# Performance work log

Hardware: AMD Instinct MI355X
Metric: run time of the kernel (lower is better)

Reference implementation:

```python
import jax, jax.numpy as jnp
import numpy as np

EPS = 1e-8


def setup_inputs() -> dict:
    key = jax.random.key(0)
    k1, k2, k3 = jax.random.split(key, 3)
    K_, M, N = 2048, 512, 64
    x = jax.random.normal(k1, (K_, M), dtype=jnp.float32)
    w_att = jax.random.uniform(k2, (M, M), dtype=jnp.float32)
    w_b = jax.random.uniform(k3, (M, N), dtype=jnp.float32)
    return {"x": x, "w_att": w_att, "w_b": w_b, "l": 8}


def reference(x, w_att, w_b, l):
    # soft attention scores over features: [k, m]
    scores_soft = jax.nn.softmax(x @ w_att, axis=-1) + EPS
    # per-target l-th largest value of w_b over the m axis -> threshold [n]
    thr = jax.lax.top_k(w_b.T, l)[0][:, -1]  # [n]
    sh = w_b - thr[None, :] + EPS  # [m, n]
    # training-phase soft hard-mask: clamp to [-1, 1], shift to [0, 1]
    scores_hard = (jnp.clip(sh, -1.0, 1.0) + 1.0) * 0.5  # [m, n]
    # outer-product combine: 'mn,km->kmn' then 'kmn,km->kmn'
    mask_weight = scores_hard[None, :, :] * scores_soft[:, :, None]  # [k, m, n]
    out = mask_weight * x[:, :, None]  # [k, m, n]
    return out, scores_hard, scores_soft, mask_weight
```

## Files before the change

kernel.cpp:

```cpp
#include <hip/hip_runtime.h>
#include <math.h>

#define K_DIM 2048
#define M_DIM 512
#define N_DIM 64
#define EPSF 1e-8f
#define ROWS 8
#define TPB 512

typedef float f32x4 __attribute__((ext_vector_type(4)));

__global__ __launch_bounds__(256) void thr_hard_kernel(
    const float* __restrict__ w_b, const int* __restrict__ lptr,
    float* __restrict__ scores_hard) {
  __shared__ float col[M_DIM];
  __shared__ float red[256];
  const int n = blockIdx.x;
  const int t = threadIdx.x;
  const int L = lptr[0];

  col[t]       = w_b[t * N_DIM + n];
  col[t + 256] = w_b[(t + 256) * N_DIM + n];
  __syncthreads();

  const float v0 = col[t], v1 = col[t + 256];
  int c0 = 0, c1 = 0;
  for (int i = 0; i < M_DIM; ++i) {
    const float c = col[i];
    c0 += (c > v0);
    c1 += (c > v1);
  }
  float cand0 = (c0 <= L - 1) ? v0 : INFINITY;
  float cand1 = (c1 <= L - 1) ? v1 : INFINITY;
  red[t] = fminf(cand0, cand1);
  __syncthreads();
  for (int s = 128; s > 0; s >>= 1) {
    if (t < s) red[t] = fminf(red[t], red[t + s]);
    __syncthreads();
  }
  const float thr = red[0];

  {
    float sh0 = (col[t] - thr) + EPSF;
    float sh1 = (col[t + 256] - thr) + EPSF;
    sh0 = fminf(fmaxf(sh0, -1.0f), 1.0f);
    sh1 = fminf(fmaxf(sh1, -1.0f), 1.0f);
    scores_hard[t * N_DIM + n]         = (sh0 + 1.0f) * 0.5f;
    scores_hard[(t + 256) * N_DIM + n] = (sh1 + 1.0f) * 0.5f;
  }
}

__global__ __launch_bounds__(TPB) void fused_kernel(
    const float* __restrict__ x, const float* __restrict__ w,
    const float* __restrict__ hard, float* __restrict__ soft,
    f32x4* __restrict__ out, f32x4* __restrict__ mw) {
  __shared__ float xs[ROWS][M_DIM];
  __shared__ float sm[ROWS][M_DIM];
  const int t = threadIdx.x;
  const int k0 = blockIdx.x * ROWS;

  {
    const f32x4* xg = (const f32x4*)(x + (size_t)k0 * M_DIM);
    f32x4* xsv = (f32x4*)&xs[0][0];
    xsv[t]       = xg[t];
    xsv[t + TPB] = xg[t + TPB];
  }
  __syncthreads();

  {
    const int half = t >> 8;
    const int j0 = t & 255;
    const int r0 = half * 4;
    float acc[4][2];
#pragma unroll
    for (int r = 0; r < 4; ++r) { acc[r][0] = 0.0f; acc[r][1] = 0.0f; }

#pragma unroll 2
    for (int m = 0; m < M_DIM; m += 4) {
      float wa[4], wb[4];
#pragma unroll
      for (int i = 0; i < 4; ++i) {
        wa[i] = w[(m + i) * M_DIM + j0];
        wb[i] = w[(m + i) * M_DIM + j0 + 256];
      }
#pragma unroll
      for (int r = 0; r < 4; ++r) {
        const float4 xv = *(const float4*)&xs[r0 + r][m];
        acc[r][0] += xv.x * wa[0] + xv.y * wa[1] + xv.z * wa[2] + xv.w * wa[3];
        acc[r][1] += xv.x * wb[0] + xv.y * wb[1] + xv.z * wb[2] + xv.w * wb[3];
      }
    }
#pragma unroll
    for (int r = 0; r < 4; ++r) {
      sm[r0 + r][j0]       = acc[r][0];
      sm[r0 + r][j0 + 256] = acc[r][1];
    }
  }
  __syncthreads();

  {
    const int r = t >> 6, ln = t & 63;
    float v[8];
    float mx = -INFINITY;
#pragma unroll
    for (int i = 0; i < 8; ++i) {
      v[i] = sm[r][ln + 64 * i];
      mx = fmaxf(mx, v[i]);
    }
#pragma unroll
    for (int s = 32; s > 0; s >>= 1) mx = fmaxf(mx, __shfl_xor(mx, s));
    float sum = 0.0f;
#pragma unroll
    for (int i = 0; i < 8; ++i) {
      v[i] = expf(v[i] - mx);
      sum += v[i];
    }
#pragma unroll
    for (int s = 32; s > 0; s >>= 1) sum += __shfl_xor(sum, s);
    const float inv = 1.0f / sum;
#pragma unroll
    for (int i = 0; i < 8; ++i) sm[r][ln + 64 * i] = v[i] * inv + EPSF;
  }
  __syncthreads();

  {
    const f32x4* smv = (const f32x4*)&sm[0][0];
    f32x4* sg = (f32x4*)(soft + (size_t)k0 * M_DIM);
    sg[t]       = smv[t];
    sg[t + TPB] = smv[t + TPB];
  }

  const f32x4* hard4 = (const f32x4*)hard;
  const size_t base = (size_t)k0 * (M_DIM * (N_DIM / 4));
#pragma unroll 4
  for (int it = 0; it < (ROWS * M_DIM * 16) / TPB; ++it) {
    const int g = it * TPB + t;
    const int q = g & 15;
    const int pair = g >> 4;
    const int m = pair & (M_DIM - 1);
    const int r = pair >> 9;
    const float ss = sm[r][m];
    const float xv = xs[r][m];
    const f32x4 sh = hard4[m * 16 + q];
    const f32x4 wgt = sh * ss;
    const f32x4 o = wgt * xv;
    out[base + g] = o;
    mw[base + g]  = wgt;
  }
}

extern "C" void kernel_launch(void* const* d_in, const int* in_sizes, int n_in,
                              void* d_out, int out_size, void* d_ws,
                              size_t ws_size, hipStream_t stream) {
  const float* x     = (const float*)d_in[0];
  const float* w_att = (const float*)d_in[1];
  const float* w_b   = (const float*)d_in[2];
  const int*   lptr  = (const int*)d_in[3];

  float* out_base = (float*)d_out;
  const size_t OUT_SZ = (size_t)K_DIM * M_DIM * N_DIM;
  float* out0 = out_base;
  float* hard = out0 + OUT_SZ;
  float* soft = hard + (size_t)M_DIM * N_DIM;
  float* mwp  = soft + (size_t)K_DIM * M_DIM;

  thr_hard_kernel<<<N_DIM, 256, 0, stream>>>(w_b, lptr, hard);
  fused_kernel<<<K_DIM / ROWS, TPB, 0, stream>>>(
      x, w_att, hard, soft, (f32x4*)out0, (f32x4*)mwp);
}
```

Baseline: 578.3 us.

## Split fused kernel into GEMM-softmax and separate broadcast combine kernel

Splits the single fused kernel into a GEMM+softmax kernel that writes soft scores to global memory and a separate combine kernel that reads soft, x and hard to write the two large outputs. The combine kernel uses 4096 blocks of 256 threads instead of 256 blocks of 512 threads, which spreads the store-bound write phase across more of the GPU and writes out and mask_weight in two separate streaming passes. The cost is an extra kernel launch and re-reading soft and x from global memory or cache.

```diff
diff --git a/kernel.cpp b/kernel.cpp
--- a/kernel.cpp
+++ b/kernel.cpp
@@ -50,10 +50,9 @@
   }
 }
 
-__global__ __launch_bounds__(TPB) void fused_kernel(
+__global__ __launch_bounds__(TPB) void gemm_softmax_kernel(
     const float* __restrict__ x, const float* __restrict__ w,
-    const float* __restrict__ hard, float* __restrict__ soft,
-    f32x4* __restrict__ out, f32x4* __restrict__ mw) {
+    float* __restrict__ soft) {
   __shared__ float xs[ROWS][M_DIM];
   __shared__ float sm[ROWS][M_DIM];
   const int t = threadIdx.x;
@@ -118,34 +117,41 @@
 #pragma unroll
     for (int s = 32; s > 0; s >>= 1) sum += __shfl_xor(sum, s);
     const float inv = 1.0f / sum;
+    float* srow = soft + (size_t)(k0 + r) * M_DIM;
 #pragma unroll
-    for (int i = 0; i < 8; ++i) sm[r][ln + 64 * i] = v[i] * inv + EPSF;
+    for (int i = 0; i < 8; ++i) srow[ln + 64 * i] = v[i] * inv + EPSF;
   }
-  __syncthreads();
+}
 
-  {
-    const f32x4* smv = (const f32x4*)&sm[0][0];
-    f32x4* sg = (f32x4*)(soft + (size_t)k0 * M_DIM);
-    sg[t]       = smv[t];
-    sg[t + TPB] = smv[t + TPB];
+__global__ __launch_bounds__(256) void combine_kernel(
+    const float* __restrict__ x, const float* __restrict__ hard,
+    const float* __restrict__ soft, f32x4* __restrict__ out,
+    f32x4* __restrict__ mw) {
+  const int t = threadIdx.x;
+  const int base = blockIdx.x * 4096;
+  const f32x4* hard4 = (const f32x4*)hard;
+
+#pragma unroll 4
+  for (int it = 0; it < 16; ++it) {
+    const int g = base + it * 256 + t;
+    const int pair = g >> 4;
+    const int q = g & 15;
+    const int m = pair & (M_DIM - 1);
+    const float ss = soft[pair];
+    const float xv = x[pair];
+    const f32x4 sh = hard4[m * 16 + q];
+    out[g] = sh * (ss * xv);
   }
 
-  const f32x4* hard4 = (const f32x4*)hard;
-  const size_t base = (size_t)k0 * (M_DIM * (N_DIM / 4));
 #pragma unroll 4
-  for (int it = 0; it < (ROWS * M_DIM * 16) / TPB; ++it) {
-    const int g = it * TPB + t;
+  for (int it = 0; it < 16; ++it) {
+    const int g = base + it * 256 + t;
+    const int pair = g >> 4;
     const int q = g & 15;
-    const int pair = g >> 4;
     const int m = pair & (M_DIM - 1);
-    const int r = pair >> 9;
-    const float ss = sm[r][m];
-    const float xv = xs[r][m];
+    const float ss = soft[pair];
     const f32x4 sh = hard4[m * 16 + q];
-    const f32x4 wgt = sh * ss;
-    const f32x4 o = wgt * xv;
-    out[base + g] = o;
-    mw[base + g]  = wgt;
+    mw[g] = sh * ss;
   }
 }
 
@@ -165,6 +171,9 @@
   float* mwp  = soft + (size_t)K_DIM * M_DIM;
 
   thr_hard_kernel<<<N_DIM, 256, 0, stream>>>(w_b, lptr, hard);
-  fused_kernel<<<K_DIM / ROWS, TPB, 0, stream>>>(
-      x, w_att, hard, soft, (f32x4*)out0, (f32x4*)mwp);
+  gemm_softmax_kernel<<<K_DIM / ROWS, TPB, 0, stream>>>(x, w_att, soft);
+
+  const int total4 = K_DIM * M_DIM * (N_DIM / 4);
+  combine_kernel<<<total4 / 4096, 256, 0, stream>>>(
+      x, hard, soft, (f32x4*)out0, (f32x4*)mwp);
 }
```

Measured after the change: 610.3 us. +5.5%, slower.
